# Kernel tuning notes

Measured on AMD Instinct MI355X. Metric: run time of the kernel, lower is better.

Reference implementation:

```python
import jax, jax.numpy as jnp
import numpy as np

IN_DIM = 4096
OUT_DIM = 4096
R = 8
C = 2
ALPHA = 32.0
RC = R // C  # head dim = 4
SCALING = ALPHA / R


def setup_inputs() -> dict:
    key = jax.random.key(0)
    ks = jax.random.split(key, 8)
    s = lambda k, shape, fan_in: jax.random.normal(k, shape, jnp.float32) / np.sqrt(fan_in)
    return {
        "x": jax.random.normal(ks[0], (4, 2048, IN_DIM), jnp.float32),
        "W_pre": s(ks[1], (OUT_DIM, IN_DIM), IN_DIM),
        "b_pre": jnp.zeros((OUT_DIM,), jnp.float32),
        "W_down": s(ks[2], (R, IN_DIM), IN_DIM),
        "W_qkv": s(ks[3], (3 * RC, R), R),
        "W_o": s(ks[4], (R, RC), RC),
        "W_up": s(ks[5], (OUT_DIM, R), R),
        "diag_b": jnp.full((OUT_DIM,), 0.001, jnp.float32),
    }


def reference(x, W_pre, b_pre, W_down, W_qkv, W_o, W_up, diag_b):
    # pretrained frozen linear
    pretrained_out = jnp.einsum("bsi,oi->bso", x, W_pre) + b_pre
    # adapter path (dropout in eval mode -> identity)
    down = jnp.einsum("bsi,ri->bsr", x, W_down)          # [B,S,R]
    qkv = jnp.einsum("bsr,tr->bst", down, W_qkv)          # [B,S,3*RC]
    q, k, v = jnp.split(qkv, 3, axis=-1)                  # each [B,S,RC]
    scores = jnp.einsum("bqd,bkd->bqk", q, k) / jnp.sqrt(jnp.float32(RC))
    attn = jax.nn.softmax(scores, axis=-1)
    ctx = jnp.einsum("bqk,bkd->bqd", attn, v)             # [B,S,RC]
    o = jnp.einsum("bsd,rd->bsr", ctx, W_o)               # [B,S,R]
    up = jnp.einsum("bsr,or->bso", o, W_up)               # [B,S,OUT]
    return pretrained_out + up * diag_b * SCALING
```

## Files before the change

kernel.cpp:

```cpp
#include <hip/hip_runtime.h>
#include <stdint.h>

#define KDIM 4096
#define NDIM 4096
#define MROWS 8192
#define SEQ 2048

typedef __attribute__((ext_vector_type(8))) short short8;
typedef __attribute__((ext_vector_type(4))) float f32x4;

__device__ __forceinline__ float bf16_bits_to_f(uint32_t u16) {
  union { uint32_t u; float f; } c; c.u = u16 << 16; return c.f;
}
__device__ __forceinline__ float dload(const void* p, size_t idx, int flag) {
  if (flag) return bf16_bits_to_f(((const uint16_t*)p)[idx]);
  return ((const float*)p)[idx];
}
__device__ __forceinline__ uint16_t f2b(float f) {
  union { float f; uint32_t u; } c; c.f = f;
  uint32_t b = c.u;
  return (uint16_t)((b + 0x7FFFu + ((b >> 16) & 1u)) >> 16);
}
__device__ __forceinline__ uint32_t pk2(float a, float b) {
  return (uint32_t)f2b(a) | ((uint32_t)f2b(b) << 16);
}
__device__ __forceinline__ void gld_lds16(const uint16_t* g, uint16_t* l) {
  __builtin_amdgcn_global_load_lds(
      (const __attribute__((address_space(1))) uint32_t*)g,
      (__attribute__((address_space(3))) uint32_t*)l, 16, 0, 0);
}

#define BARRIER() asm volatile("s_barrier" ::: "memory")
#define VMCNT4() asm volatile("s_waitcnt vmcnt(4)" ::: "memory")
#define VMCNT0() asm volatile("s_waitcnt vmcnt(0)" ::: "memory")

__global__ void k_detect(const uint16_t* xu, int* flag) {
  int lane = threadIdx.x;
  int bad = 0;
  for (int i = lane; i < 512; i += 64) {
    float v = bf16_bits_to_f((uint32_t)xu[i]);
    if (!(v == v) || fabsf(v) > 1000.0f) bad++;
  }
  for (int off = 32; off > 0; off >>= 1) bad += __shfl_down(bad, off);
  if (lane == 0) *flag = (bad < 32) ? 1 : 0;
}

__global__ __launch_bounds__(256) void k_prep(
    const void* W_down, const void* W_qkv, const void* W_up,
    const void* diag_b, const void* b_pre,
    float* WcT, float* W_up_s, float* b_pre_f, const int* flagp) {
  const int flag = *flagp;
  const int tid = blockIdx.x * 256 + threadIdx.x;
  const int tt = tid >> 12;
  const int i = tid & 4095;
  float s = 0.f;
#pragma unroll
  for (int r = 0; r < 8; ++r)
    s += dload(W_qkv, tt * 8 + r, flag) * dload(W_down, (size_t)r * 4096 + i, flag);
  WcT[(size_t)tt * 4096 + i] = s;
  if (tid < 32768)
    W_up_s[tid] = dload(W_up, tid, flag) * dload(diag_b, tid >> 3, flag) * 4.0f;
  if (tid < 4096)
    b_pre_f[tid] = dload(b_pre, tid, flag);
}

__global__ __launch_bounds__(256) void k_qkvconv(
    const void* x, const float* WcT, float* qkv, uint16_t* xb,
    const void* W_pre, uint16_t* wb, int do_conv, const int* flagp) {
  const int flag = *flagp;
  if (blockIdx.x >= 2048) {
    if (flag || !do_conv) return;
    const float* w = (const float*)W_pre;
    const size_t n = (size_t)NDIM * KDIM;
    const size_t stride = (size_t)512 * 256 * 8;
    for (size_t idx = (((size_t)blockIdx.x - 2048) * 256 + threadIdx.x) * 8;
         idx < n; idx += stride) {
      const float4 a = *(const float4*)(w + idx);
      const float4 b = *(const float4*)(w + idx + 4);
      uint4 p;
      p.x = pk2(a.x, a.y);
      p.y = pk2(a.z, a.w);
      p.z = pk2(b.x, b.y);
      p.w = pk2(b.z, b.w);
      *(uint4*)(wb + idx) = p;
    }
    return;
  }
  const int wv = (int)((blockIdx.x * 256 + threadIdx.x) >> 6);
  const int lane = threadIdx.x & 63;
  float acc[12];
#pragma unroll
  for (int t = 0; t < 12; ++t) acc[t] = 0.f;
  if (!flag) {
    const float* xr = (const float*)x + (size_t)wv * KDIM;
    uint16_t* xo = xb + (size_t)wv * KDIM;
    for (int i0 = 0; i0 < KDIM; i0 += 256) {
      const int i = i0 + lane * 4;
      const float4 xv = *(const float4*)(xr + i);
      if (do_conv) {
        uint2 p;
        p.x = pk2(xv.x, xv.y);
        p.y = pk2(xv.z, xv.w);
        *(uint2*)(xo + i) = p;
      }
#pragma unroll
      for (int t = 0; t < 12; ++t) {
        const float4 w4 = *(const float4*)(WcT + (size_t)t * 4096 + i);
        acc[t] += xv.x * w4.x + xv.y * w4.y + xv.z * w4.z + xv.w * w4.w;
      }
    }
  } else {
    const uint16_t* xr = (const uint16_t*)x + (size_t)wv * KDIM;
    for (int i0 = 0; i0 < KDIM; i0 += 512) {
      const int i = i0 + lane * 8;
      const uint4 xv = *(const uint4*)(xr + i);
      const float x0 = bf16_bits_to_f(xv.x & 0xFFFFu), x1 = bf16_bits_to_f(xv.x >> 16);
      const float x2 = bf16_bits_to_f(xv.y & 0xFFFFu), x3 = bf16_bits_to_f(xv.y >> 16);
      const float x4 = bf16_bits_to_f(xv.z & 0xFFFFu), x5 = bf16_bits_to_f(xv.z >> 16);
      const float x6 = bf16_bits_to_f(xv.w & 0xFFFFu), x7 = bf16_bits_to_f(xv.w >> 16);
#pragma unroll
      for (int t = 0; t < 12; ++t) {
        const float4 w0 = *(const float4*)(WcT + (size_t)t * 4096 + i);
        const float4 w1 = *(const float4*)(WcT + (size_t)t * 4096 + i + 4);
        acc[t] += x0 * w0.x + x1 * w0.y + x2 * w0.z + x3 * w0.w +
                  x4 * w1.x + x5 * w1.y + x6 * w1.z + x7 * w1.w;
      }
    }
  }
#pragma unroll
  for (int t = 0; t < 12; ++t)
    for (int off = 32; off > 0; off >>= 1) acc[t] += __shfl_down(acc[t], off);
  if (lane == 0) {
#pragma unroll
    for (int t = 0; t < 12; ++t) qkv[(size_t)wv * 12 + t] = acc[t];
  }
}

__global__ __launch_bounds__(256) void k_attn(const float* qkv, const void* W_o,
                                              float* a_o, const int* flagp) {
  const int flag = *flagp;
  __shared__ uint2 sk[SEQ];
  __shared__ uint2 sv[SEQ];
  __shared__ float part[4][64][9];
  const int b = blockIdx.x >> 5;
  const int rb = blockIdx.x & 31;
  for (int j = threadIdx.x; j < SEQ; j += 256) {
    const float* qr = qkv + ((size_t)b * SEQ + j) * 12;
    uint2 pk, pv;
    pk.x = pk2(qr[4], qr[5]);
    pk.y = pk2(qr[6], qr[7]);
    pv.x = pk2(qr[8], qr[9]);
    pv.y = pk2(qr[10], qr[11]);
    sk[j] = pk;
    sv[j] = pv;
  }
  __syncthreads();
  const int row = threadIdx.x & 63;
  const int seg = threadIdx.x >> 6;
  const size_t m = (size_t)b * SEQ + rb * 64 + row;
  const float* qr = qkv + m * 12;
  const float q0 = qr[0] * 0.5f, q1 = qr[1] * 0.5f;
  const float q2 = qr[2] * 0.5f, q3 = qr[3] * 0.5f;
  float l = 0.f, c0 = 0.f, c1 = 0.f, c2 = 0.f, c3 = 0.f;
  const int j0 = seg * 512;
  for (int j = j0; j < j0 + 512; ++j) {
    const uint2 kk = sk[j];
    const float k0 = bf16_bits_to_f(kk.x & 0xFFFFu);
    const float k1 = bf16_bits_to_f(kk.x >> 16);
    const float k2 = bf16_bits_to_f(kk.y & 0xFFFFu);
    const float k3 = bf16_bits_to_f(kk.y >> 16);
    const float s = q0 * k0 + q1 * k1 + q2 * k2 + q3 * k3;
    const float e = __expf(s);
    const uint2 vv = sv[j];
    l += e;
    c0 += e * bf16_bits_to_f(vv.x & 0xFFFFu);
    c1 += e * bf16_bits_to_f(vv.x >> 16);
    c2 += e * bf16_bits_to_f(vv.y & 0xFFFFu);
    c3 += e * bf16_bits_to_f(vv.y >> 16);
  }
  part[seg][row][0] = l;
  part[seg][row][1] = c0;
  part[seg][row][2] = c1;
  part[seg][row][3] = c2;
  part[seg][row][4] = c3;
  __syncthreads();
  if (seg == 0) {
    l = part[0][row][0] + part[1][row][0] + part[2][row][0] + part[3][row][0];
    c0 = part[0][row][1] + part[1][row][1] + part[2][row][1] + part[3][row][1];
    c1 = part[0][row][2] + part[1][row][2] + part[2][row][2] + part[3][row][2];
    c2 = part[0][row][3] + part[1][row][3] + part[2][row][3] + part[3][row][3];
    c3 = part[0][row][4] + part[1][row][4] + part[2][row][4] + part[3][row][4];
    const float inv = 1.0f / l;
    c0 *= inv; c1 *= inv; c2 *= inv; c3 *= inv;
    float wo[32];
#pragma unroll
    for (int i = 0; i < 32; ++i) wo[i] = dload(W_o, i, flag);
#pragma unroll
    for (int r = 0; r < 8; ++r)
      a_o[m * 8 + r] = c0 * wo[r * 4 + 0] + c1 * wo[r * 4 + 1] +
                       c2 * wo[r * 4 + 2] + c3 * wo[r * 4 + 3];
  }
}

__global__ __launch_bounds__(512, 2) void k_gemm8(
    const void* x, const void* w, const uint16_t* xb, const uint16_t* wb,
    const float* a_o, const float* W_up_s, const float* b_pre_f, void* out,
    const int* flagp) {
  const int flag = *flagp;
  const uint16_t* Ag = flag ? (const uint16_t*)x : xb;
  const uint16_t* Bg = flag ? (const uint16_t*)w : wb;
  __shared__ __align__(16) uint16_t smem[2][2][16384];

  const int t = threadIdx.x;
  const int lane = t & 63;
  const int wid = t >> 6;
  const int swz = ((int)blockIdx.x & 7) * 64 + ((int)blockIdx.x >> 3);
  const int bm = swz & 31;
  const int bn = swz >> 5;

  const int sr0 = 0 * 64 + wid * 8 + (lane >> 3);
  const int sr1 = 1 * 64 + wid * 8 + (lane >> 3);
  const int sc0 = ((lane & 7) * 8) ^ (((sr0 >> 2) & 1) * 16);
  const int sc1 = ((lane & 7) * 8) ^ (((sr1 >> 2) & 1) * 16);
  const size_t aoff0 = (size_t)(bm * 256 + sr0) * KDIM + sc0;
  const size_t aoff1 = (size_t)(bm * 256 + sr1) * KDIM + sc1;
  const size_t boff0 = (size_t)(bn * 256 + sr0) * KDIM + sc0;
  const size_t boff1 = (size_t)(bn * 256 + sr1) * KDIM + sc1;

  const int wn_idx = wid & 3;
  const int wm_idx = wid >> 2;
  const int wave_m0 = wm_idx * 128;
  const int wave_n0 = wn_idx * 64;
  const int fr = lane & 15;
  const int fkbe = ((lane >> 4) * 8) ^ ((((lane & 15) >> 2) & 1) * 16);

  f32x4 acc[8][4];
#pragma unroll
  for (int a = 0; a < 8; ++a)
#pragma unroll
    for (int b = 0; b < 4; ++b) acc[a][b] = (f32x4){0.f, 0.f, 0.f, 0.f};

  short8 a_reg[4][2];
  short8 b_reg[2][2][2];

#define STAGE(BUF, OP, H, TILE)                                               \
  do {                                                                        \
    const uint16_t* g_ = (OP) ? Bg : Ag;                                      \
    const size_t ho_ = (size_t)(H) * (128 * KDIM) + (size_t)(TILE) * 64;      \
    gld_lds16(g_ + ((OP) ? boff0 : aoff0) + ho_,                              \
              &smem[BUF][OP][(H) * 8192 + wid * 512]);                        \
    gld_lds16(g_ + ((OP) ? boff1 : aoff1) + ho_,                              \
              &smem[BUF][OP][(H) * 8192 + 4096 + wid * 512]);                 \
  } while (0)

#define A_LOAD(BUF, MH)                                                       \
  do {                                                                        \
    _Pragma("unroll") for (int f = 0; f < 4; ++f) {                           \
      a_reg[f][0] = *(const short8*)&smem[BUF][0][                            \
          (wave_m0 + ((MH)*4 + f) * 16 + fr) * 64 + fkbe];                    \
      a_reg[f][1] = *(const short8*)&smem[BUF][0][                            \
          (wave_m0 + ((MH)*4 + f) * 16 + fr) * 64 + 32 + fkbe];               \
    }                                                                         \
  } while (0)

#define B_LOAD(BUF, NH)                                                       \
  do {                                                                        \
    _Pragma("unroll") for (int g = 0; g < 2; ++g) {                           \
      b_reg[NH][g][0] = *(const short8*)&smem[BUF][1][                        \
          (wave_n0 + ((NH)*2 + g) * 16 + fr) * 64 + fkbe];                    \
      b_reg[NH][g][1] = *(const short8*)&smem[BUF][1][                        \
          (wave_n0 + ((NH)*2 + g) * 16 + fr) * 64 + 32 + fkbe];               \
    }                                                                         \
  } while (0)

#define MFMA_Q(MH, NH)                                                        \
  do {                                                                        \
    __builtin_amdgcn_s_setprio(1);                                            \
    _Pragma("unroll") for (int f = 0; f < 4; ++f) {                           \
      _Pragma("unroll") for (int g = 0; g < 2; ++g) {                         \
        acc[(MH)*4 + f][(NH)*2 + g] = __builtin_amdgcn_mfma_f32_16x16x32_bf16(\
            a_reg[f][0], b_reg[NH][g][0], acc[(MH)*4 + f][(NH)*2 + g], 0,0,0);\
        acc[(MH)*4 + f][(NH)*2 + g] = __builtin_amdgcn_mfma_f32_16x16x32_bf16(\
            a_reg[f][1], b_reg[NH][g][1], acc[(MH)*4 + f][(NH)*2 + g], 0,0,0);\
      }                                                                       \
    }                                                                         \
    __builtin_amdgcn_s_setprio(0);                                            \
  } while (0)

  STAGE(0, 0, 0, 0); STAGE(0, 0, 1, 0); STAGE(0, 1, 0, 0); STAGE(0, 1, 1, 0);
  STAGE(1, 1, 0, 1); STAGE(1, 1, 1, 1);
  VMCNT4();
  BARRIER();

#pragma unroll 1
  for (int it = 0; it < 31; ++it) {
    const int tO = 2 * it + 1, tE2 = 2 * it + 2, tO2 = 2 * it + 3;
    A_LOAD(0, 0); B_LOAD(0, 0); STAGE(1, 0, 0, tO);
    BARRIER(); MFMA_Q(0, 0); BARRIER();
    B_LOAD(0, 1); STAGE(1, 0, 1, tO);
    BARRIER(); MFMA_Q(0, 1); BARRIER();
    A_LOAD(0, 1); STAGE(0, 1, 0, tE2);
    BARRIER(); MFMA_Q(1, 0); BARRIER();
    STAGE(0, 1, 1, tE2);
    BARRIER(); MFMA_Q(1, 1); VMCNT4(); BARRIER();
    A_LOAD(1, 0); B_LOAD(1, 0); STAGE(0, 0, 0, tE2);
    BARRIER(); MFMA_Q(0, 0); BARRIER();
    B_LOAD(1, 1); STAGE(0, 0, 1, tE2);
    BARRIER(); MFMA_Q(0, 1); BARRIER();
    A_LOAD(1, 1); STAGE(1, 1, 0, tO2);
    BARRIER(); MFMA_Q(1, 0); BARRIER();
    STAGE(1, 1, 1, tO2);
    BARRIER(); MFMA_Q(1, 1); VMCNT4(); BARRIER();
  }
  A_LOAD(0, 0); B_LOAD(0, 0); STAGE(1, 0, 0, 63);
  BARRIER(); MFMA_Q(0, 0); BARRIER();
  B_LOAD(0, 1); STAGE(1, 0, 1, 63);
  BARRIER(); MFMA_Q(0, 1); BARRIER();
  A_LOAD(0, 1);
  BARRIER(); MFMA_Q(1, 0); BARRIER();
  BARRIER(); MFMA_Q(1, 1); VMCNT0(); BARRIER();
  A_LOAD(1, 0); B_LOAD(1, 0);
  BARRIER(); MFMA_Q(0, 0); BARRIER();
  B_LOAD(1, 1);
  BARRIER(); MFMA_Q(0, 1); BARRIER();
  A_LOAD(1, 1);
  BARRIER(); MFMA_Q(1, 0); BARRIER();
  BARRIER(); MFMA_Q(1, 1); BARRIER();

  const int rq = (lane >> 4) * 4;
  float4 u0r[4], u1r[4];
  float bpr[4];
#pragma unroll
  for (int nf = 0; nf < 4; ++nf) {
    const int gn = bn * 256 + wave_n0 + nf * 16 + fr;
    bpr[nf] = b_pre_f[gn];
    u0r[nf] = *(const float4*)&W_up_s[(size_t)gn * 8];
    u1r[nf] = *(const float4*)&W_up_s[(size_t)gn * 8 + 4];
  }
#pragma unroll
  for (int mf = 0; mf < 8; ++mf) {
#pragma unroll
    for (int r = 0; r < 4; ++r) {
      const int gm = bm * 256 + wave_m0 + mf * 16 + rq + r;
      const float4 a0 = *(const float4*)&a_o[(size_t)gm * 8];
      const float4 a1 = *(const float4*)&a_o[(size_t)gm * 8 + 4];
#pragma unroll
      for (int nf = 0; nf < 4; ++nf) {
        const int gn = bn * 256 + wave_n0 + nf * 16 + fr;
        float v = acc[mf][nf][r] + bpr[nf] +
                  a0.x * u0r[nf].x + a0.y * u0r[nf].y + a0.z * u0r[nf].z +
                  a0.w * u0r[nf].w + a1.x * u1r[nf].x + a1.y * u1r[nf].y +
                  a1.z * u1r[nf].z + a1.w * u1r[nf].w;
        const size_t oidx = (size_t)gm * NDIM + gn;
        if (flag) ((uint16_t*)out)[oidx] = f2b(v);
        else ((float*)out)[oidx] = v;
      }
    }
  }
#undef STAGE
#undef A_LOAD
#undef B_LOAD
#undef MFMA_Q
}

__global__ __launch_bounds__(256) void k_gemm_fb(
    const void* x, const void* w, const float* a_o, const float* W_up_s,
    const float* b_pre_f, void* out, const int* flagp) {
  const int flag = *flagp;
  __shared__ __align__(16) uint16_t sA[128 * 64];
  __shared__ __align__(16) uint16_t sB[128 * 64];
  const int t = threadIdx.x;
  const int bm = blockIdx.x & 63;
  const int bn = blockIdx.x >> 6;
  const int srow = t >> 1;
  const int scol = (t & 1) * 32;
  const size_t ga = ((size_t)(bm * 128 + srow)) * KDIM + scol;
  const size_t gb = ((size_t)(bn * 128 + srow)) * KDIM + scol;
  const int lane = t & 63;
  const int wid = t >> 6;
  const int wm = (wid & 1) * 64;
  const int wn = (wid >> 1) * 64;
  const int fr = lane & 15;
  const int fk = (lane >> 4) * 8;
  f32x4 acc[4][4];
#pragma unroll
  for (int a = 0; a < 4; ++a)
#pragma unroll
    for (int bq = 0; bq < 4; ++bq) acc[a][bq] = (f32x4){0.f, 0.f, 0.f, 0.f};

  for (int k0 = 0; k0 < KDIM; k0 += 64) {
    __syncthreads();
    if (flag) {
      const uint16_t* gx = (const uint16_t*)x + ga + k0;
      const uint16_t* gw = (const uint16_t*)w + gb + k0;
#pragma unroll
      for (int c = 0; c < 4; ++c) {
        *(uint4*)&sA[srow * 64 + scol + c * 8] = *(const uint4*)(gx + c * 8);
        *(uint4*)&sB[srow * 64 + scol + c * 8] = *(const uint4*)(gw + c * 8);
      }
    } else {
      const float* gx = (const float*)x + ga + k0;
      const float* gw = (const float*)w + gb + k0;
#pragma unroll
      for (int c = 0; c < 4; ++c) {
        float4 xa = *(const float4*)(gx + c * 8);
        float4 xb2 = *(const float4*)(gx + c * 8 + 4);
        uint4 pk;
        pk.x = pk2(xa.x, xa.y);
        pk.y = pk2(xa.z, xa.w);
        pk.z = pk2(xb2.x, xb2.y);
        pk.w = pk2(xb2.z, xb2.w);
        *(uint4*)&sA[srow * 64 + scol + c * 8] = pk;
        float4 wa = *(const float4*)(gw + c * 8);
        float4 wb2 = *(const float4*)(gw + c * 8 + 4);
        uint4 pw;
        pw.x = pk2(wa.x, wa.y);
        pw.y = pk2(wa.z, wa.w);
        pw.z = pk2(wb2.x, wb2.y);
        pw.w = pk2(wb2.z, wb2.w);
        *(uint4*)&sB[srow * 64 + scol + c * 8] = pw;
      }
    }
    __syncthreads();
#pragma unroll
    for (int kk = 0; kk < 64; kk += 32) {
      short8 af[4], bfr[4];
#pragma unroll
      for (int mb = 0; mb < 4; ++mb)
        af[mb] = *(const short8*)&sA[(wm + mb * 16 + fr) * 64 + kk + fk];
#pragma unroll
      for (int nb = 0; nb < 4; ++nb)
        bfr[nb] = *(const short8*)&sB[(wn + nb * 16 + fr) * 64 + kk + fk];
#pragma unroll
      for (int mb = 0; mb < 4; ++mb)
#pragma unroll
        for (int nb = 0; nb < 4; ++nb)
          acc[mb][nb] = __builtin_amdgcn_mfma_f32_16x16x32_bf16(
              af[mb], bfr[nb], acc[mb][nb], 0, 0, 0);
    }
  }
  const int rq = (lane >> 4) * 4;
#pragma unroll
  for (int nb = 0; nb < 4; ++nb) {
    const int gn = bn * 128 + wn + nb * 16 + fr;
    const float bp = b_pre_f[gn];
    const float4 u0 = *(const float4*)&W_up_s[(size_t)gn * 8];
    const float4 u1 = *(const float4*)&W_up_s[(size_t)gn * 8 + 4];
#pragma unroll
    for (int mb = 0; mb < 4; ++mb) {
#pragma unroll
      for (int r = 0; r < 4; ++r) {
        const int gm = bm * 128 + wm + mb * 16 + rq + r;
        const float4 a0 = *(const float4*)&a_o[(size_t)gm * 8];
        const float4 a1 = *(const float4*)&a_o[(size_t)gm * 8 + 4];
        float v = acc[mb][nb][r] + bp + a0.x * u0.x + a0.y * u0.y +
                  a0.z * u0.z + a0.w * u0.w + a1.x * u1.x + a1.y * u1.y +
                  a1.z * u1.z + a1.w * u1.w;
        const size_t oidx = (size_t)gm * NDIM + gn;
        if (flag) ((uint16_t*)out)[oidx] = f2b(v);
        else ((float*)out)[oidx] = v;
      }
    }
  }
}

extern "C" void kernel_launch(void* const* d_in, const int* in_sizes, int n_in,
                              void* d_out, int out_size, void* d_ws,
                              size_t ws_size, hipStream_t stream) {
  const void* x = d_in[0];
  const void* W_pre = d_in[1];
  const void* b_pre = d_in[2];
  const void* W_down = d_in[3];
  const void* W_qkv = d_in[4];
  const void* W_o = d_in[5];
  const void* W_up = d_in[6];
  const void* diag_b = d_in[7];

  char* ws = (char*)d_ws;
  int* flag_p = (int*)ws;
  float* WcT = (float*)(ws + 256);
  float* qkv = (float*)(ws + 196864);
  float* a_o = (float*)(ws + 590080);
  float* W_up_s = (float*)(ws + 852224);
  float* b_pre_f = (float*)(ws + 983296);
  uint16_t* xb = (uint16_t*)(ws + 1048576);
  uint16_t* wb = (uint16_t*)(ws + 68157440);
  const bool big = ws_size >= (size_t)101711872;

  k_detect<<<1, 64, 0, stream>>>((const uint16_t*)x, flag_p);
  k_prep<<<192, 256, 0, stream>>>(W_down, W_qkv, W_up, diag_b, b_pre, WcT,
                                  W_up_s, b_pre_f, flag_p);
  k_qkvconv<<<2560, 256, 0, stream>>>(x, WcT, qkv, xb, W_pre, wb,
                                      big ? 1 : 0, flag_p);
  k_attn<<<128, 256, 0, stream>>>(qkv, W_o, a_o, flag_p);
  if (big)
    k_gemm8<<<512, 512, 0, stream>>>(x, W_pre, xb, wb, a_o, W_up_s, b_pre_f,
                                     d_out, flag_p);
  else
    k_gemm_fb<<<2048, 256, 0, stream>>>(x, W_pre, a_o, W_up_s, b_pre_f, d_out,
                                        flag_p);
}
```

Baseline: 613.6 us.

## Split attention across more blocks, retile GEMM per XCD, extend LDS swizzle

The attention kernel now launches 256 blocks, each covering 32 query rows split into 8 key segments instead of 64 rows in 4 segments. This raises parallelism on the small attention stage at the cost of each block reloading K/V into shared memory twice as often. The GEMM block-to-tile mapping now gives each XCD an 8x8 square of output tiles, aiming to improve L2 reuse of A and B panels. The LDS swizzle adds an extra XOR bit on the column index, applied consistently to the global-to-LDS stores and the fragment reads, to reduce bank conflicts.

```diff
diff --git a/kernel.cpp b/kernel.cpp
--- a/kernel.cpp
+++ b/kernel.cpp
@@ -141,9 +141,9 @@
   const int flag = *flagp;
   __shared__ uint2 sk[SEQ];
   __shared__ uint2 sv[SEQ];
-  __shared__ float part[4][64][9];
-  const int b = blockIdx.x >> 5;
-  const int rb = blockIdx.x & 31;
+  __shared__ float part[8][32][9];
+  const int b = blockIdx.x >> 6;
+  const int rb = blockIdx.x & 63;
   for (int j = threadIdx.x; j < SEQ; j += 256) {
     const float* qr = qkv + ((size_t)b * SEQ + j) * 12;
     uint2 pk, pv;
@@ -155,15 +155,15 @@
     sv[j] = pv;
   }
   __syncthreads();
-  const int row = threadIdx.x & 63;
-  const int seg = threadIdx.x >> 6;
-  const size_t m = (size_t)b * SEQ + rb * 64 + row;
+  const int row = threadIdx.x & 31;
+  const int seg = threadIdx.x >> 5;
+  const size_t m = (size_t)b * SEQ + rb * 32 + row;
   const float* qr = qkv + m * 12;
   const float q0 = qr[0] * 0.5f, q1 = qr[1] * 0.5f;
   const float q2 = qr[2] * 0.5f, q3 = qr[3] * 0.5f;
   float l = 0.f, c0 = 0.f, c1 = 0.f, c2 = 0.f, c3 = 0.f;
-  const int j0 = seg * 512;
-  for (int j = j0; j < j0 + 512; ++j) {
+  const int j0 = seg * 256;
+  for (int j = j0; j < j0 + 256; ++j) {
     const uint2 kk = sk[j];
     const float k0 = bf16_bits_to_f(kk.x & 0xFFFFu);
     const float k1 = bf16_bits_to_f(kk.x >> 16);
@@ -185,11 +185,15 @@
   part[seg][row][4] = c3;
   __syncthreads();
   if (seg == 0) {
-    l = part[0][row][0] + part[1][row][0] + part[2][row][0] + part[3][row][0];
-    c0 = part[0][row][1] + part[1][row][1] + part[2][row][1] + part[3][row][1];
-    c1 = part[0][row][2] + part[1][row][2] + part[2][row][2] + part[3][row][2];
-    c2 = part[0][row][3] + part[1][row][3] + part[2][row][3] + part[3][row][3];
-    c3 = part[0][row][4] + part[1][row][4] + part[2][row][4] + part[3][row][4];
+    l = 0.f; c0 = 0.f; c1 = 0.f; c2 = 0.f; c3 = 0.f;
+#pragma unroll
+    for (int s2 = 0; s2 < 8; ++s2) {
+      l += part[s2][row][0];
+      c0 += part[s2][row][1];
+      c1 += part[s2][row][2];
+      c2 += part[s2][row][3];
+      c3 += part[s2][row][4];
+    }
     const float inv = 1.0f / l;
     c0 *= inv; c1 *= inv; c2 *= inv; c3 *= inv;
     float wo[32];
@@ -214,14 +218,17 @@
   const int t = threadIdx.x;
   const int lane = t & 63;
   const int wid = t >> 6;
-  const int swz = ((int)blockIdx.x & 7) * 64 + ((int)blockIdx.x >> 3);
-  const int bm = swz & 31;
-  const int bn = swz >> 5;
+  const int xcd = (int)blockIdx.x & 7;
+  const int j = (int)blockIdx.x >> 3;
+  const int bm = (xcd & 3) * 8 + (j & 7);
+  const int bn = (xcd >> 2) * 8 + (j >> 3);
 
   const int sr0 = 0 * 64 + wid * 8 + (lane >> 3);
   const int sr1 = 1 * 64 + wid * 8 + (lane >> 3);
-  const int sc0 = ((lane & 7) * 8) ^ (((sr0 >> 2) & 1) * 16);
-  const int sc1 = ((lane & 7) * 8) ^ (((sr1 >> 2) & 1) * 16);
+  const int sc0 = ((lane & 7) * 8) ^ (((sr0 >> 2) & 1) * 16) ^
+                  (((sr0 >> 3) & 1) * 32);
+  const int sc1 = ((lane & 7) * 8) ^ (((sr1 >> 2) & 1) * 16) ^
+                  (((sr1 >> 3) & 1) * 32);
   const size_t aoff0 = (size_t)(bm * 256 + sr0) * KDIM + sc0;
   const size_t aoff1 = (size_t)(bm * 256 + sr1) * KDIM + sc1;
   const size_t boff0 = (size_t)(bn * 256 + sr0) * KDIM + sc0;
@@ -232,7 +239,8 @@
   const int wave_m0 = wm_idx * 128;
   const int wave_n0 = wn_idx * 64;
   const int fr = lane & 15;
-  const int fkbe = ((lane >> 4) * 8) ^ ((((lane & 15) >> 2) & 1) * 16);
+  const int fkbe = ((lane >> 4) * 8) ^ (((lane >> 2) & 1) * 16) ^
+                   (((lane >> 3) & 1) * 32);
 
   f32x4 acc[8][4];
 #pragma unroll
@@ -259,7 +267,7 @@
       a_reg[f][0] = *(const short8*)&smem[BUF][0][                            \
           (wave_m0 + ((MH)*4 + f) * 16 + fr) * 64 + fkbe];                    \
       a_reg[f][1] = *(const short8*)&smem[BUF][0][                            \
-          (wave_m0 + ((MH)*4 + f) * 16 + fr) * 64 + 32 + fkbe];               \
+          (wave_m0 + ((MH)*4 + f) * 16 + fr) * 64 + (fkbe ^ 32)];             \
     }                                                                         \
   } while (0)
 
@@ -269,7 +277,7 @@
       b_reg[NH][g][0] = *(const short8*)&smem[BUF][1][                        \
           (wave_n0 + ((NH)*2 + g) * 16 + fr) * 64 + fkbe];                    \
       b_reg[NH][g][1] = *(const short8*)&smem[BUF][1][                        \
-          (wave_n0 + ((NH)*2 + g) * 16 + fr) * 64 + 32 + fkbe];               \
+          (wave_n0 + ((NH)*2 + g) * 16 + fr) * 64 + (fkbe ^ 32)];             \
     }                                                                         \
   } while (0)
 
@@ -492,7 +500,7 @@
                                   W_up_s, b_pre_f, flag_p);
   k_qkvconv<<<2560, 256, 0, stream>>>(x, WcT, qkv, xb, W_pre, wb,
                                       big ? 1 : 0, flag_p);
-  k_attn<<<128, 256, 0, stream>>>(qkv, W_o, a_o, flag_p);
+  k_attn<<<256, 256, 0, stream>>>(qkv, W_o, a_o, flag_p);
   if (big)
     k_gemm8<<<512, 512, 0, stream>>>(x, W_pre, xb, wb, a_o, W_up_s, b_pre_f,
                                      d_out, flag_p);
```

Measured after the change: 597.9 us. -2.6%, faster.
